# Kernel optimization log

Hardware: AMD Instinct MI355X
Metric: run time of the kernel (lower is better)

Reference implementation:

```python
import jax, jax.numpy as jnp
import numpy as np

EPS = 1e-5

def _act_quant(x):
    # per-token int8 absmax quantization with STE passthrough
    s = 127.0 / jnp.clip(jnp.max(jnp.abs(x), axis=-1, keepdims=True), EPS, None)
    xq = jnp.clip(jnp.round(x * s), -128.0, 127.0) / s
    return x + jax.lax.stop_gradient(xq - x)

def _weight_quant(w):
    # ternary {-1,0,1} abs-mean quantization with STE passthrough
    s = 1.0 / jnp.clip(jnp.mean(jnp.abs(w)), EPS, None)
    wq = jnp.clip(jnp.round(w * s), -1.0, 1.0) / s
    return w + jax.lax.stop_gradient(wq - w)

def bitlinear(x, w, b=None):
    y = _act_quant(x) @ _weight_quant(w).T
    return y if b is None else y + b

def setup_inputs() -> dict:
    key = jax.random.key(0)
    ks = jax.random.split(key, 6)
    B, T, C = 64, 256, 1024
    std = 1.0 / np.sqrt(C)
    return {
        "x": jax.random.normal(ks[0], (B, T, C), dtype=jnp.float32),
        "Wq": jax.random.normal(ks[1], (C, C), dtype=jnp.float32) * std,
        "Wk": jax.random.normal(ks[2], (C, C), dtype=jnp.float32) * std,
        "Wv": jax.random.normal(ks[3], (C, C), dtype=jnp.float32) * std,
        "Wp": jax.random.normal(ks[4], (C, C), dtype=jnp.float32) * std,
        "bp": jnp.zeros((C,), dtype=jnp.float32),
        "n_head": 16,
    }

def reference(x, Wq, Wk, Wv, Wp, bp, n_head):
    B, T, C = x.shape
    hd = C // n_head
    def heads(t):  # [B,T,C] -> [B,H,T,hd]
        return t.reshape(B, T, n_head, hd).transpose(0, 2, 1, 3)
    q = heads(bitlinear(x, Wq))
    k = heads(bitlinear(x, Wk))
    v = heads(bitlinear(x, Wv))
    attn = jnp.einsum("bhqd,bhkd->bhqk", q, k) * (1.0 / np.sqrt(hd))
    causal = jnp.tril(jnp.ones((T, T), dtype=bool))
    attn = jnp.where(causal, attn, -jnp.inf)
    attn = jax.nn.softmax(attn, axis=-1)
    y = jnp.einsum("bhqk,bhkd->bhqd", attn, v)
    y = y.transpose(0, 2, 1, 3).reshape(B, T, C)
    return bitlinear(y, Wp, bp)
```

## Files before the change

### kernel.cpp

```cpp
#include <hip/hip_runtime.h>
#include <math.h>

#define AS1 __attribute__((address_space(1)))
#define AS3 __attribute__((address_space(3)))

typedef unsigned short u16;
typedef signed char i8;
typedef short bf16x8 __attribute__((ext_vector_type(8)));
typedef float f32x4 __attribute__((ext_vector_type(4)));
typedef int i32x4 __attribute__((ext_vector_type(4)));

static constexpr int BB = 64, T = 256, C = 1024, H = 16, HD = 64;
static constexpr int M = BB * T;
static constexpr float EPSF = 1e-5f;

static constexpr size_t W8_OFF   = 0;
static constexpr size_t XQ8_OFF  = 4ull  << 20;
static constexpr size_t RSX_OFF  = 20ull << 20;
static constexpr size_t RSY_OFF  = (20ull << 20) + (64 << 10);
static constexpr size_t WSUM_OFF = (20ull << 20) + (128 << 10);
static constexpr size_t WPART_OFF= WSUM_OFF + 64;
static constexpr size_t QB_OFF   = 21ull << 20;
static constexpr size_t KB_OFF   = 53ull << 20;
static constexpr size_t VT_OFF   = 85ull << 20;

__device__ __forceinline__ u16 f2bf_rne(float f) {
    unsigned x = __float_as_uint(f);
    unsigned r = x + 0x7FFF + ((x >> 16) & 1);
    return (u16)(r >> 16);
}

__global__ __launch_bounds__(256) void wsum1_kernel(const float* __restrict__ Wq,
    const float* __restrict__ Wk, const float* __restrict__ Wv,
    const float* __restrict__ Wp, double* __restrict__ wpart)
{
    const int mat = blockIdx.x >> 6;
    const float* W = (mat == 0) ? Wq : (mat == 1) ? Wk : (mat == 2) ? Wv : Wp;
    const int t = threadIdx.x;
    const int base = (blockIdx.x & 63) * 256 + t;
    double s = 0.0;
    for (int i = 0; i < 64; ++i) s += (double)fabsf(W[base + (i << 14)]);
    #pragma unroll
    for (int off = 32; off >= 1; off >>= 1) s += __shfl_down(s, off);
    __shared__ double red[4];
    if ((t & 63) == 0) red[t >> 6] = s;
    __syncthreads();
    if (t == 0) wpart[blockIdx.x] = red[0] + red[1] + red[2] + red[3];
}

__global__ __launch_bounds__(256) void wsum2_kernel(const double* __restrict__ wpart,
                                                    double* __restrict__ wsum)
{
    const int t = threadIdx.x;
    double s = wpart[t];
    #pragma unroll
    for (int off = 32; off >= 1; off >>= 1) s += __shfl_down(s, off);
    if ((t & 63) == 0) wsum[t >> 6] = s;
}

__global__ __launch_bounds__(256) void wquant_kernel(const float* __restrict__ Wq,
    const float* __restrict__ Wk, const float* __restrict__ Wv,
    const float* __restrict__ Wp, const double* __restrict__ wsum,
    i8* __restrict__ w8)
{
    const int mat = blockIdx.x >> 8;
    const float* W = (mat == 0) ? Wq : (mat == 1) ? Wk : (mat == 2) ? Wv : Wp;
    const float mean = (float)(wsum[mat] * (1.0 / 1048576.0));
    const float s = 1.0f / fmaxf(mean, EPSF);
    const int g = (blockIdx.x & 255) * 256 + threadIdx.x;
    const int lane = g & 63, kt = (g >> 6) & 15, nt = g >> 10;
    const int row = nt * 16 + (lane & 15);
    const int k0 = kt * 64 + (lane >> 4) * 16;
    const float* src = W + (size_t)row * 1024 + k0;
    union { i8 b[16]; i32x4 v; } o;
    #pragma unroll
    for (int j = 0; j < 16; ++j)
        o.b[j] = (i8)(int)fminf(fmaxf(rintf(src[j] * s), -1.f), 1.f);
    *(i32x4*)(w8 + ((size_t)mat << 20) + (size_t)g * 16) = o.v;
}

__global__ __launch_bounds__(256) void actquant_kernel(const float* __restrict__ x,
    i8* __restrict__ xq, float* __restrict__ rs)
{
    const int row = blockIdx.x;
    const int t = threadIdx.x;
    float4 v = ((const float4*)(x + (size_t)row * C))[t];
    float m = fmaxf(fmaxf(fabsf(v.x), fabsf(v.y)), fmaxf(fabsf(v.z), fabsf(v.w)));
    #pragma unroll
    for (int off = 32; off >= 1; off >>= 1) m = fmaxf(m, __shfl_down(m, off));
    __shared__ float red[4];
    if ((t & 63) == 0) red[t >> 6] = m;
    __syncthreads();
    float mm = fmaxf(fmaxf(red[0], red[1]), fmaxf(red[2], red[3]));
    mm = fmaxf(mm, EPSF);
    const float s = 127.0f / mm;
    if (t == 0) rs[row] = mm / 127.0f;
    char4 o;
    o.x = (i8)(int)fminf(fmaxf(rintf(v.x * s), -128.f), 127.f);
    o.y = (i8)(int)fminf(fmaxf(rintf(v.y * s), -128.f), 127.f);
    o.z = (i8)(int)fminf(fmaxf(rintf(v.z * s), -128.f), 127.f);
    o.w = (i8)(int)fminf(fmaxf(rintf(v.w * s), -128.f), 127.f);
    ((char4*)(xq + (size_t)row * C))[t] = o;
}

template<bool QKV, int NNB>
__global__ __launch_bounds__(256, 2) void gemm_kernel(const i8* __restrict__ A,
    const i8* __restrict__ w8, const float* __restrict__ rs_row,
    const double* __restrict__ wsum, u16* __restrict__ qb, u16* __restrict__ kb,
    u16* __restrict__ vt, float* __restrict__ outp, const float* __restrict__ bias)
{
    constexpr int K = 1024, N = 1024;
    constexpr int NT = 16;
    __shared__ __align__(16) i8 Asm[4][128 * 64];

    const int t = threadIdx.x;

    const int nwg = NNB * 128;
    const int wg = (int)blockIdx.x;
    const int swz = (wg & 7) * (nwg >> 3) + (wg >> 3);
    const int mb = swz / NNB, nb = swz % NNB;
    const int m0 = mb * 128;
    const int mat = QKV ? (nb >> 2) : 3;
    const int n0m = QKV ? ((nb & 3) * 256) : (nb * 256);
    const i8* Bw = w8 + ((size_t)mat << 20);

    const int lane = t & 63, wn = t >> 6;
    const int mr = lane & 15, quad = lane >> 4;

    const int g1 = t, g2 = t + 256;
    const int L1 = (g1 * 16) ^ (((g1 >> 3) & 7) << 4);
    const int L2 = (g2 * 16) ^ (((g2 >> 3) & 7) << 4);
    const i8* a1 = A + (size_t)(m0 + (L1 >> 6)) * K + (L1 & 63);
    const i8* a2 = A + (size_t)(m0 + (L2 >> 6)) * K + (L2 & 63);

    const int vvs = (mr >> 1) & 7;
    int aoff[8];
    #pragma unroll
    for (int m = 0; m < 8; ++m)
        aoff[m] = ((m * 16 + mr) * 64 + quad * 16) ^ (vvs << 4);

    const int ntb = (n0m >> 4) + wn * 4;
    const i8* bfp = Bw + (size_t)ntb * 16384 + (size_t)lane * 16;

    i32x4 acc[8][4];
    #pragma unroll
    for (int m = 0; m < 8; ++m)
        #pragma unroll
        for (int n = 0; n < 4; ++n) acc[m][n] = (i32x4){0, 0, 0, 0};

    #pragma unroll
    for (int p = 0; p < 2; ++p) {
        const int k0 = p * 64;
        __builtin_amdgcn_global_load_lds((const AS1 void*)(a1 + k0), (AS3 void*)&Asm[p][g1 * 16], 16, 0, 0);
        __builtin_amdgcn_global_load_lds((const AS1 void*)(a2 + k0), (AS3 void*)&Asm[p][g2 * 16], 16, 0, 0);
    }
    asm volatile("s_waitcnt vmcnt(2)" ::: "memory");
    __builtin_amdgcn_s_barrier();
    __builtin_amdgcn_sched_barrier(0);

    for (int tt = 0; tt < NT; ++tt) {
        const i8* Ac = Asm[tt & 3];
        i8* An = Asm[(tt + 2) & 3];
        const int kn = (tt + 2) * 64;

        i32x4 bf[4];
        #pragma unroll
        for (int n = 0; n < 4; ++n)
            bf[n] = *(const i32x4*)(bfp + (size_t)n * 16384 + tt * 1024);

        if (tt < NT - 2) {
            __builtin_amdgcn_global_load_lds((const AS1 void*)(a1 + kn), (AS3 void*)&An[g1 * 16], 16, 0, 0);
            __builtin_amdgcn_global_load_lds((const AS1 void*)(a2 + kn), (AS3 void*)&An[g2 * 16], 16, 0, 0);
        }

        i32x4 af[8];
        #pragma unroll
        for (int m = 0; m < 8; ++m) af[m] = *(const i32x4*)&Ac[aoff[m]];

        __builtin_amdgcn_s_setprio(1);
        #pragma unroll
        for (int m = 0; m < 8; ++m)
            #pragma unroll
            for (int n = 0; n < 4; ++n)
                acc[m][n] = __builtin_amdgcn_mfma_i32_16x16x64_i8(af[m], bf[n], acc[m][n], 0, 0, 0);
        __builtin_amdgcn_s_setprio(0);

        if (tt < NT - 2) {
            asm volatile("s_waitcnt vmcnt(2)" ::: "memory");
        } else if (tt < NT - 1) {
            asm volatile("s_waitcnt vmcnt(0)" ::: "memory");
        }
        __builtin_amdgcn_s_barrier();
        __builtin_amdgcn_sched_barrier(0);
    }

    float wsc = fmaxf((float)(wsum[mat] * (1.0 / 1048576.0)), EPSF);
    if (QKV && mat == 0) wsc *= 0.125f;

    if (QKV && mat == 2) {
        #pragma unroll
        for (int m = 0; m < 8; ++m) {
            const int gr0 = m0 + m * 16 + quad * 4;
            const int bbi = gr0 >> 8, tl = gr0 & 255;
            const float4 rs4 = *(const float4*)(rs_row + gr0);
            #pragma unroll
            for (int n = 0; n < 4; ++n) {
                const int gcol = n0m + wn * 64 + n * 16 + mr;
                ushort4 o;
                o.x = f2bf_rne((float)acc[m][n][0] * rs4.x * wsc);
                o.y = f2bf_rne((float)acc[m][n][1] * rs4.y * wsc);
                o.z = f2bf_rne((float)acc[m][n][2] * rs4.z * wsc);
                o.w = f2bf_rne((float)acc[m][n][3] * rs4.w * wsc);
                *(ushort4*)(vt + (size_t)(bbi * 1024 + gcol) * 256 + tl) = o;
            }
        }
        return;
    }

    u16* ob = QKV ? ((mat == 0) ? qb : kb) : nullptr;
    #pragma unroll
    for (int m = 0; m < 8; ++m) {
        const int gr0 = m0 + m * 16 + quad * 4;
        #pragma unroll
        for (int r = 0; r < 4; ++r) {
            const int grow = gr0 + r;
            const float sc = rs_row[grow] * wsc;
            #pragma unroll
            for (int n = 0; n < 4; ++n) {
                const int gcol = n0m + wn * 64 + n * 16 + mr;
                const float val = (float)acc[m][n][r] * sc;
                if (QKV) {
                    ob[(size_t)grow * N + gcol] = f2bf_rne(val);
                } else {
                    outp[(size_t)grow * N + gcol] = val + bias[gcol];
                }
            }
        }
    }
}

__global__ __launch_bounds__(256) void attn_kernel(const u16* __restrict__ qb,
    const u16* __restrict__ kb, const u16* __restrict__ vt, float* __restrict__ y)
{
    const int t = threadIdx.x;
    const int qt = 3 - (int)(blockIdx.x >> 10);
    const int bh = blockIdx.x & 1023;
    const int b = bh >> 4, h = bh & 15;
    const int w = t >> 6, lane = t & 63;
    const int cl = lane & 15, quad = lane >> 4;
    const size_t gb = (size_t)(b * T) * 1024 + h * 64;
    const u16* vtb = vt + (size_t)(b * 1024 + h * 64) * 256;

    const int qrow = qt * 64 + w * 16;
    const int jtiles = (qrow >> 4) + 1;

    const u16* qrp = qb + gb + (size_t)(qrow + cl) * 1024 + quad * 8;
    bf16x8 qf0 = *(const bf16x8*)qrp;
    bf16x8 qf1 = *(const bf16x8*)(qrp + 32);

    f32x4 Sp[16];
    #pragma unroll
    for (int i2 = 0; i2 < 16; ++i2) Sp[i2] = (f32x4){0.f, 0.f, 0.f, 0.f};

    const u16* krp = kb + gb + (size_t)cl * 1024 + quad * 8;
    #pragma unroll
    for (int jt = 0; jt < 16; ++jt) {
        if (jt < jtiles) {
            const u16* kp = krp + (size_t)(jt * 16) * 1024;
            bf16x8 kf0 = *(const bf16x8*)kp;
            bf16x8 kf1 = *(const bf16x8*)(kp + 32);
            Sp[jt] = __builtin_amdgcn_mfma_f32_16x16x32_bf16(kf0, qf0, Sp[jt], 0, 0, 0);
            Sp[jt] = __builtin_amdgcn_mfma_f32_16x16x32_bf16(kf1, qf1, Sp[jt], 0, 0, 0);
            if (jt == jtiles - 1) {
                #pragma unroll
                for (int r = 0; r < 4; ++r)
                    if (quad * 4 + r > cl) Sp[jt][r] = -INFINITY;
            }
        }
    }

    float mx = -INFINITY;
    #pragma unroll
    for (int jt = 0; jt < 16; ++jt) if (jt < jtiles) {
        #pragma unroll
        for (int r = 0; r < 4; ++r) mx = fmaxf(mx, Sp[jt][r]);
    }
    mx = fmaxf(mx, __shfl_xor(mx, 16));
    mx = fmaxf(mx, __shfl_xor(mx, 32));
    float l = 0.f;
    #pragma unroll
    for (int jt = 0; jt < 16; ++jt) if (jt < jtiles) {
        #pragma unroll
        for (int r = 0; r < 4; ++r) {
            float p = __expf(Sp[jt][r] - mx);
            Sp[jt][r] = p;
            l += p;
        }
    }
    l += __shfl_xor(l, 16);
    l += __shfl_xor(l, 32);

    f32x4 O[4];
    #pragma unroll
    for (int i2 = 0; i2 < 4; ++i2) O[i2] = (f32x4){0.f, 0.f, 0.f, 0.f};

    const int s01 = ((quad & 1) << 5) + cl;
    const bool lo = quad < 2;
    #pragma unroll
    for (int jc = 0; jc < 8; ++jc) {
        if (jc * 2 < jtiles) {
            int pk[2][2];
            #pragma unroll
            for (int s = 0; s < 2; ++s) {
                const f32x4 v = Sp[jc * 2 + s];
                pk[s][0] = (int)((unsigned)f2bf_rne(v[0]) | ((unsigned)f2bf_rne(v[1]) << 16));
                pk[s][1] = (int)((unsigned)f2bf_rne(v[2]) | ((unsigned)f2bf_rne(v[3]) << 16));
            }
            int a0 = __shfl(pk[0][0], s01),      a1 = __shfl(pk[0][1], s01);
            int a2 = __shfl(pk[0][0], s01 + 16), a3 = __shfl(pk[0][1], s01 + 16);
            int b0 = __shfl(pk[1][0], s01),      b1 = __shfl(pk[1][1], s01);
            int b2 = __shfl(pk[1][0], s01 + 16), b3 = __shfl(pk[1][1], s01 + 16);
            union { int i[4]; bf16x8 v; } af;
            af.i[0] = lo ? a0 : b0;
            af.i[1] = lo ? a1 : b1;
            af.i[2] = lo ? a2 : b2;
            af.i[3] = lo ? a3 : b3;
            const u16* vp = vtb + (size_t)cl * 256 + jc * 32 + quad * 8;
            #pragma unroll
            for (int dt = 0; dt < 4; ++dt) {
                bf16x8 vf = *(const bf16x8*)(vp + (size_t)dt * 16 * 256);
                O[dt] = __builtin_amdgcn_mfma_f32_16x16x32_bf16(af.v, vf, O[dt], 0, 0, 0);
            }
        }
    }

    float inv[4];
    #pragma unroll
    for (int r = 0; r < 4; ++r) inv[r] = 1.0f / __shfl(l, quad * 4 + r);
    #pragma unroll
    for (int dt = 0; dt < 4; ++dt)
        #pragma unroll
        for (int r = 0; r < 4; ++r)
            y[gb + (size_t)(qrow + quad * 4 + r) * 1024 + dt * 16 + cl] = O[dt][r] * inv[r];
}

extern "C" void kernel_launch(void* const* d_in, const int* in_sizes, int n_in,
                              void* d_out, int out_size, void* d_ws, size_t ws_size,
                              hipStream_t stream) {
    (void)in_sizes; (void)n_in; (void)out_size; (void)ws_size;
    const float* x  = (const float*)d_in[0];
    const float* Wq = (const float*)d_in[1];
    const float* Wk = (const float*)d_in[2];
    const float* Wv = (const float*)d_in[3];
    const float* Wp = (const float*)d_in[4];
    const float* bp = (const float*)d_in[5];
    float* out = (float*)d_out;
    char* ws = (char*)d_ws;

    i8*     w8   = (i8*)(ws + W8_OFF);
    i8*     xq8  = (i8*)(ws + XQ8_OFF);
    float*  rsx  = (float*)(ws + RSX_OFF);
    float*  rsy  = (float*)(ws + RSY_OFF);
    double* wsum = (double*)(ws + WSUM_OFF);
    double* wpart= (double*)(ws + WPART_OFF);
    u16*    qb   = (u16*)(ws + QB_OFF);
    u16*    kb   = (u16*)(ws + KB_OFF);
    u16*    vt   = (u16*)(ws + VT_OFF);

    wsum1_kernel<<<256, 256, 0, stream>>>(Wq, Wk, Wv, Wp, wpart);
    wsum2_kernel<<<1, 256, 0, stream>>>(wpart, wsum);
    wquant_kernel<<<1024, 256, 0, stream>>>(Wq, Wk, Wv, Wp, wsum, w8);
    actquant_kernel<<<M, 256, 0, stream>>>(x, xq8, rsx);

    gemm_kernel<true, 12><<<1536, 256, 0, stream>>>(xq8, w8, rsx, wsum, qb, kb, vt, nullptr, nullptr);

    attn_kernel<<<4 * 1024, 256, 0, stream>>>(qb, kb, vt, out);

    actquant_kernel<<<M, 256, 0, stream>>>(out, xq8, rsy);
    gemm_kernel<false, 4><<<512, 256, 0, stream>>>(xq8, w8, rsy, wsum, nullptr, nullptr, nullptr, out, bp);
}
```

Baseline: 307.3 us.

## Stage K and V panels into LDS via async global_load_lds in attention

```diff
diff --git a/kernel.cpp b/kernel.cpp
--- a/kernel.cpp
+++ b/kernel.cpp
@@ -242,6 +242,7 @@
 __global__ __launch_bounds__(256) void attn_kernel(const u16* __restrict__ qb,
     const u16* __restrict__ kb, const u16* __restrict__ vt, float* __restrict__ y)
 {
+    __shared__ __align__(16) i8 panel[32768];
     const int t = threadIdx.x;
     const int qt = 3 - (int)(blockIdx.x >> 10);
     const int bh = blockIdx.x & 1023;
@@ -249,7 +250,19 @@
     const int w = t >> 6, lane = t & 63;
     const int cl = lane & 15, quad = lane >> 4;
     const size_t gb = (size_t)(b * T) * 1024 + h * 64;
-    const u16* vtb = vt + (size_t)(b * 1024 + h * 64) * 256;
+    const char* kpb = (const char*)(kb + gb);
+    const char* vpb = (const char*)(vt + (size_t)(b * 1024 + h * 64) * 256);
+
+    const int jtB   = qt * 4 + 4;
+    const int jtB16 = jtB << 4;
+    const int jtB256= jtB << 8;
+
+    #pragma unroll
+    for (int cc = 0; cc < 8; ++cc)
+        for (int rr = t; rr < jtB16; rr += 256)
+            __builtin_amdgcn_global_load_lds(
+                (const AS1 void*)(kpb + (size_t)rr * 2048 + cc * 16),
+                (AS3 void*)&panel[cc * jtB256 + rr * 16], 16, 0, 0);
 
     const int qrow = qt * 64 + w * 16;
     const int jtiles = (qrow >> 4) + 1;
@@ -258,17 +271,19 @@
     bf16x8 qf0 = *(const bf16x8*)qrp;
     bf16x8 qf1 = *(const bf16x8*)(qrp + 32);
 
+    asm volatile("s_waitcnt vmcnt(0)" ::: "memory");
+    __syncthreads();
+
     f32x4 Sp[16];
     #pragma unroll
     for (int i2 = 0; i2 < 16; ++i2) Sp[i2] = (f32x4){0.f, 0.f, 0.f, 0.f};
 
-    const u16* krp = kb + gb + (size_t)cl * 1024 + quad * 8;
     #pragma unroll
     for (int jt = 0; jt < 16; ++jt) {
         if (jt < jtiles) {
-            const u16* kp = krp + (size_t)(jt * 16) * 1024;
-            bf16x8 kf0 = *(const bf16x8*)kp;
-            bf16x8 kf1 = *(const bf16x8*)(kp + 32);
+            const i8* kp0 = &panel[quad * jtB256 + (jt * 16 + cl) * 16];
+            bf16x8 kf0 = *(const bf16x8*)kp0;
+            bf16x8 kf1 = *(const bf16x8*)(kp0 + 4 * jtB256);
             Sp[jt] = __builtin_amdgcn_mfma_f32_16x16x32_bf16(kf0, qf0, Sp[jt], 0, 0, 0);
             Sp[jt] = __builtin_amdgcn_mfma_f32_16x16x32_bf16(kf1, qf1, Sp[jt], 0, 0, 0);
             if (jt == jtiles - 1) {
@@ -279,6 +294,16 @@
         }
     }
 
+    __syncthreads();
+
+    {
+        const int nv = jtB << 7;
+        for (int g = t; g < nv; g += 256)
+            __builtin_amdgcn_global_load_lds(
+                (const AS1 void*)(vpb + (size_t)(g & 63) * 512 + (g >> 6) * 16),
+                (AS3 void*)&panel[g * 16], 16, 0, 0);
+    }
+
     float mx = -INFINITY;
     #pragma unroll
     for (int jt = 0; jt < 16; ++jt) if (jt < jtiles) {
@@ -299,6 +324,9 @@
     }
     l += __shfl_xor(l, 16);
     l += __shfl_xor(l, 32);
+
+    asm volatile("s_waitcnt vmcnt(0)" ::: "memory");
+    __syncthreads();
 
     f32x4 O[4];
     #pragma unroll
@@ -325,10 +353,10 @@
             af.i[1] = lo ? a1 : b1;
             af.i[2] = lo ? a2 : b2;
             af.i[3] = lo ? a3 : b3;
-            const u16* vp = vtb + (size_t)cl * 256 + jc * 32 + quad * 8;
+            const i8* vp = &panel[(4 * jc + quad) * 1024 + cl * 16];
             #pragma unroll
             for (int dt = 0; dt < 4; ++dt) {
-                bf16x8 vf = *(const bf16x8*)(vp + (size_t)dt * 16 * 256);
+                bf16x8 vf = *(const bf16x8*)(vp + dt * 256);
                 O[dt] = __builtin_amdgcn_mfma_f32_16x16x32_bf16(af.v, vf, O[dt], 0, 0, 0);
             }
         }
```

Result: faster. 287.3 us (-6.5%).
